# Performance work log

Measured on AMD Instinct MI355X. Metric: run time of the kernel, lower is better.

## Reference

```python
import jax, jax.numpy as jnp
import numpy as np

# Arbitrary non-contiguous kernel tap offsets (constructor arg sk_ind)
SK_IND = np.array([-512, -256, -128, -96, -64, -48, -32, -24, -16, -12, -8, -6,
                   -4, -3, -2, -1, 0, 1, 2, 3, 4, 6, 8, 12, 16, 24, 32, 48,
                   64, 96, 128, 256], dtype=np.int32)
IN_CHANNELS = 64
OUT_CHANNELS = 64
BATCH = 16
INPUT_LEN = 4096


def setup_inputs() -> dict:
    key = jax.random.key(0)
    k1, k2 = jax.random.split(key)
    x = jax.random.normal(k1, (BATCH, IN_CHANNELS, INPUT_LEN), dtype=jnp.float32)
    sk_weights = jax.random.normal(k2, (OUT_CHANNELS, IN_CHANNELS, SK_IND.shape[0]), dtype=jnp.float32)
    return {"x": x, "sk_weights": sk_weights}


def reference(x, sk_weights):
    # x: [B, Cin, L]; sk_weights: [Cout, Cin, K]
    B, C, L = x.shape
    low_pad = max(-int(SK_IND.min()), 0)   # zeros consumed by negative taps
    high_pad = max(int(SK_IND.max()), 0)   # zeros consumed by positive taps
    # Original pads zeros AFTER the signal: [x, zeros(high_pad), zeros(low_pad)];
    # negative numpy indices then wrap into the trailing low_pad zeros.
    padded = jnp.concatenate([x, jnp.zeros((B, C, high_pad + low_pad), x.dtype)], axis=-1)
    padded_len = L + high_pad + low_pad
    idx = SK_IND[:, None] + np.arange(L)                 # [K, L], static
    idx = np.where(idx < 0, padded_len + idx, idx)       # emulate numpy negative-index wrap
    gathered = padded[:, :, idx]                          # [B, Cin, K, L]
    # Per-position GEMM: contract over (Cin, K)
    return jnp.einsum('oik,bikl->bol', sk_weights, gathered)  # [B, Cout, L]
```

## Files before the change

kernel.cpp:

```cpp
#include <hip/hip_runtime.h>


#define B_    16
#define CIN   64
#define COUT  64
#define LEN   4096
#define PAD_LO 512
#define PAD_HI 256
#define LPAD  (LEN + PAD_LO + PAD_HI)
#define NTAP  32

typedef float f32x4 __attribute__((ext_vector_type(4)));
typedef short bf16x8_s __attribute__((ext_vector_type(8)));
typedef __bf16 bf16x8_b __attribute__((ext_vector_type(8)));
typedef unsigned short u16x8 __attribute__((ext_vector_type(8)));

template <typename V>
static __device__ inline auto mfma_16x16x32_bf16(V a, V b, f32x4 c, int)
    -> decltype(__builtin_amdgcn_mfma_f32_16x16x32_bf16(a, b, c, 0, 0, 0)) {
  return __builtin_amdgcn_mfma_f32_16x16x32_bf16(a, b, c, 0, 0, 0);
}
template <typename V>
static __device__ inline f32x4 mfma_16x16x32_bf16(V a, V b, f32x4 c, long) {
  return __builtin_amdgcn_mfma_f32_16x16x32_bf16(
      __builtin_bit_cast(bf16x8_b, a), __builtin_bit_cast(bf16x8_b, b), c, 0, 0, 0);
}

static __device__ inline unsigned short f32_to_bf16_rne(float f) {
  unsigned int u = __builtin_bit_cast(unsigned int, f);
  u += 0x7fffu + ((u >> 16) & 1u);
  return (unsigned short)(u >> 16);
}

static __device__ inline void async_copy16(const void* g, void* l) {
  __builtin_amdgcn_global_load_lds((const __attribute__((address_space(1))) unsigned int*)g,
                                   (__attribute__((address_space(3))) unsigned int*)l, 16, 0, 0);
}

__global__ __launch_bounds__(256) void prep_xw(const float* __restrict__ x,
                                               const float* __restrict__ w,
                                               unsigned short* __restrict__ xp,
                                               unsigned short* __restrict__ wf) {
  __shared__ float tile[64][65];
  const int id = blockIdx.x;
  const int b = 2 * (id & 7) + ((id >> 3) & 1);
  const int xt = id >> 4;
  const int lp0 = xt * 64;
  const int tid = threadIdx.x;
  const bool data = (lp0 >= PAD_LO) && (lp0 < PAD_LO + LEN);
  if (data) {
    const int l0 = lp0 - PAD_LO;
#pragma unroll
    for (int it = 0; it < 4; ++it) {
      const int pidx = it * 256 + tid;
      const int il = pidx >> 4;
      const int lq = (pidx & 15) * 4;
      const float4 v = *(const float4*)&x[(size_t)(b * CIN + il) * LEN + l0 + lq];
      tile[lq + 0][il] = v.x;
      tile[lq + 1][il] = v.y;
      tile[lq + 2][il] = v.z;
      tile[lq + 3][il] = v.w;
    }
  } else if (lp0 < PAD_LO) {
    const int base = (b * 8 + xt) * 1024;
#pragma unroll
    for (int it = 0; it < 4; ++it) {
      const int e = base + it * 256 + tid;
      const int j = e & 7;
      const int lane = (e >> 3) & 63;
      const int m = (e >> 9) & 3;
      const int c = (e >> 11) & 1;
      const int t = e >> 12;
      const int o = m * 16 + (lane & 15);
      const int i = c * 32 + (lane >> 4) * 8 + j;
      wf[e] = f32_to_bf16_rne(w[(size_t)(o * CIN + i) * NTAP + t]);
    }
  }
  __syncthreads();
#pragma unroll
  for (int it = 0; it < 2; ++it) {
    const int pidx = it * 256 + tid;
    const int ll = pidx >> 3;
    const int i8 = (pidx & 7) * 8;
    u16x8 v = {0, 0, 0, 0, 0, 0, 0, 0};
    if (data) {
#pragma unroll
      for (int j = 0; j < 8; ++j) v[j] = f32_to_bf16_rne(tile[ll][i8 + j]);
    }
    *(u16x8*)&xp[(size_t)(b * LPAD + lp0 + ll) * CIN + i8] = v;
  }
}

__global__ __launch_bounds__(512, 2) void sconv_main(const unsigned short* __restrict__ xp,
                                                     const unsigned short* __restrict__ wf,
                                                     float* __restrict__ out) {
  constexpr int TAP[NTAP] = {-512, -256, -128, -96, -64, -48, -32, -24, -16, -12, -8,
                             -6,   -4,   -3,   -2,  -1,  0,   1,   2,   3,   4,  6,
                             8,    12,   16,   24,  32,  48,  64,  96,  128, 256};
  __shared__ alignas(16) char smem[131072];

  const int id = blockIdx.x;
  const int b = (id & 7) * 2 + (id >> 7);
  const int l0 = ((id >> 3) & 15) * 256;
  const int lb = l0 + PAD_LO;
  const int tid = threadIdx.x;
  const int wv = tid >> 6, lane = tid & 63;
  const int q = lane >> 4, r = lane & 15;
  const int lh = wv >> 1, ch = wv & 1;

  const char* xbase = (const char*)xp + ((size_t)b * LPAD + lb) * (CIN * 2);
  const char* wbase = (const char*)wf;

  bf16x8_s Wreg[2][4], Breg[2][4];
  f32x4 acc[4][4] = {};

  auto loadW = [&](int tt, int p) {
    const char* src = wbase + tt * 8192 + ch * 4096 + lane * 16;
#pragma unroll
    for (int m = 0; m < 4; ++m)
      Wreg[p][m] = *(const bf16x8_s*)(src + m * 1024);
  };
  auto readB = [&](int tt, int p) {
    const int e = (TAP[tt] + r) & 7;
#pragma unroll
    for (int n = 0; n < 4; ++n) {
      const int slot = (lb + TAP[tt] + lh * 64 + 16 * n + r) & 1023;
      Breg[p][n] = *(const bf16x8_s*)(smem + slot * 128 + (((ch * 4 + q) ^ e) << 4));
    }
  };

#pragma unroll
  for (int i = 0; i < 16; ++i) {
    const int g = wv + i * 8;
    const int ra = -512 + g * 8 + (lane >> 3);
    const int cs = (lane & 7) ^ (ra & 7);
    const int sb = (lb - 512 + g * 8) & 1023;
    async_copy16(xbase + (ptrdiff_t)ra * 128 + cs * 16, smem + sb * 128);
  }
  loadW(0, 0);
  __syncthreads();
  readB(0, 0);

#pragma unroll
  for (int t = 0; t < NTAP; ++t) {
    const int p = t & 1;
    if (t + 1 < NTAP) {
      loadW(t + 1, p ^ 1);
      readB(t + 1, p ^ 1);
    }
    __builtin_amdgcn_sched_barrier(0);
#pragma unroll
    for (int m = 0; m < 4; ++m)
#pragma unroll
      for (int n = 0; n < 4; ++n)
        acc[m][n] = mfma_16x16x32_bf16(Wreg[p][m], Breg[p][n], acc[m][n], 0);
  }

  __syncthreads();
  if (ch == 1) {
#pragma unroll
    for (int m = 0; m < 4; ++m)
#pragma unroll
      for (int n = 0; n < 4; ++n)
        *(f32x4*)(smem + lh * 16384 + ((m * 4 + n) * 64 + lane) * 16) = acc[m][n];
  }
  __syncthreads();
  if (ch == 0) {
#pragma unroll
    for (int m = 0; m < 4; ++m)
#pragma unroll
      for (int n = 0; n < 4; ++n) {
        const f32x4 other = *(const f32x4*)(smem + lh * 16384 + ((m * 4 + n) * 64 + lane) * 16);
        const f32x4 v = acc[m][n] + other;
#pragma unroll
        for (int d = 0; d < 4; ++d) {
          const int o = 16 * m + 4 * q + d;
          const int l = l0 + lh * 64 + 16 * n + r;
          out[((size_t)b * COUT + o) * LEN + l] = v[d];
        }
      }
  }
}

extern "C" void kernel_launch(void* const* d_in, const int* in_sizes, int n_in,
                              void* d_out, int out_size, void* d_ws, size_t ws_size,
                              hipStream_t stream) {
  const float* x = (const float*)d_in[0];
  const float* w = (const float*)d_in[1];
  float* out = (float*)d_out;

  unsigned short* xp = (unsigned short*)d_ws;
  unsigned short* wfp = xp + (size_t)B_ * LPAD * CIN;

  prep_xw<<<dim3((LPAD / 64) * B_), 256, 0, stream>>>(x, w, xp, wfp);
  sconv_main<<<dim3(256), 512, 0, stream>>>(xp, wfp, out);
}
```

Before: 88.93 us.

## Fuse x transpose and bf16 conversion into main conv kernel staging

The padded, transposed bf16 copy of x is no longer built in the prep kernel. The main kernel now reads fp32 x directly, converts it to bf16 and writes the swizzled LDS window itself, zero-filling out-of-range rows. Part of the staging (rows ahead of the window) is interleaved with the first tap iterations and followed by a barrier. This removes a full global write and re-read of the transposed x buffer, in exchange for synchronous scalar LDS stores and fp32 loads inside the main kernel.

```diff
diff --git a/kernel.cpp b/kernel.cpp
--- a/kernel.cpp
+++ b/kernel.cpp
@@ -5,15 +5,11 @@
 #define CIN   64
 #define COUT  64
 #define LEN   4096
-#define PAD_LO 512
-#define PAD_HI 256
-#define LPAD  (LEN + PAD_LO + PAD_HI)
 #define NTAP  32
 
 typedef float f32x4 __attribute__((ext_vector_type(4)));
 typedef short bf16x8_s __attribute__((ext_vector_type(8)));
 typedef __bf16 bf16x8_b __attribute__((ext_vector_type(8)));
-typedef unsigned short u16x8 __attribute__((ext_vector_type(8)));
 
 template <typename V>
 static __device__ inline auto mfma_16x16x32_bf16(V a, V b, f32x4 c, int)
@@ -32,66 +28,24 @@
   return (unsigned short)(u >> 16);
 }
 
-static __device__ inline void async_copy16(const void* g, void* l) {
-  __builtin_amdgcn_global_load_lds((const __attribute__((address_space(1))) unsigned int*)g,
-                                   (__attribute__((address_space(3))) unsigned int*)l, 16, 0, 0);
-}
-
-__global__ __launch_bounds__(256) void prep_xw(const float* __restrict__ x,
-                                               const float* __restrict__ w,
-                                               unsigned short* __restrict__ xp,
-                                               unsigned short* __restrict__ wf) {
-  __shared__ float tile[64][65];
-  const int id = blockIdx.x;
-  const int b = 2 * (id & 7) + ((id >> 3) & 1);
-  const int xt = id >> 4;
-  const int lp0 = xt * 64;
-  const int tid = threadIdx.x;
-  const bool data = (lp0 >= PAD_LO) && (lp0 < PAD_LO + LEN);
-  if (data) {
-    const int l0 = lp0 - PAD_LO;
+__global__ __launch_bounds__(256) void prep_w(const float* __restrict__ w,
+                                              unsigned short* __restrict__ wf) {
+  const int base = blockIdx.x * 1024;
 #pragma unroll
-    for (int it = 0; it < 4; ++it) {
-      const int pidx = it * 256 + tid;
-      const int il = pidx >> 4;
-      const int lq = (pidx & 15) * 4;
-      const float4 v = *(const float4*)&x[(size_t)(b * CIN + il) * LEN + l0 + lq];
-      tile[lq + 0][il] = v.x;
-      tile[lq + 1][il] = v.y;
-      tile[lq + 2][il] = v.z;
-      tile[lq + 3][il] = v.w;
-    }
-  } else if (lp0 < PAD_LO) {
-    const int base = (b * 8 + xt) * 1024;
-#pragma unroll
-    for (int it = 0; it < 4; ++it) {
-      const int e = base + it * 256 + tid;
-      const int j = e & 7;
-      const int lane = (e >> 3) & 63;
-      const int m = (e >> 9) & 3;
-      const int c = (e >> 11) & 1;
-      const int t = e >> 12;
-      const int o = m * 16 + (lane & 15);
-      const int i = c * 32 + (lane >> 4) * 8 + j;
-      wf[e] = f32_to_bf16_rne(w[(size_t)(o * CIN + i) * NTAP + t]);
-    }
-  }
-  __syncthreads();
-#pragma unroll
-  for (int it = 0; it < 2; ++it) {
-    const int pidx = it * 256 + tid;
-    const int ll = pidx >> 3;
-    const int i8 = (pidx & 7) * 8;
-    u16x8 v = {0, 0, 0, 0, 0, 0, 0, 0};
-    if (data) {
-#pragma unroll
-      for (int j = 0; j < 8; ++j) v[j] = f32_to_bf16_rne(tile[ll][i8 + j]);
-    }
-    *(u16x8*)&xp[(size_t)(b * LPAD + lp0 + ll) * CIN + i8] = v;
+  for (int it = 0; it < 4; ++it) {
+    const int e = base + it * 256 + threadIdx.x;
+    const int j = e & 7;
+    const int lane = (e >> 3) & 63;
+    const int m = (e >> 9) & 3;
+    const int c = (e >> 11) & 1;
+    const int t = e >> 12;
+    const int o = m * 16 + (lane & 15);
+    const int i = c * 32 + (lane >> 4) * 8 + j;
+    wf[e] = f32_to_bf16_rne(w[(size_t)(o * CIN + i) * NTAP + t]);
   }
 }
 
-__global__ __launch_bounds__(512, 2) void sconv_main(const unsigned short* __restrict__ xp,
+__global__ __launch_bounds__(512, 2) void sconv_main(const float* __restrict__ x,
                                                      const unsigned short* __restrict__ wf,
                                                      float* __restrict__ out) {
   constexpr int TAP[NTAP] = {-512, -256, -128, -96, -64, -48, -32, -24, -16, -12, -8,
@@ -102,14 +56,34 @@
   const int id = blockIdx.x;
   const int b = (id & 7) * 2 + (id >> 7);
   const int l0 = ((id >> 3) & 15) * 256;
-  const int lb = l0 + PAD_LO;
+  const int lb = l0 + 512;
   const int tid = threadIdx.x;
   const int wv = tid >> 6, lane = tid & 63;
   const int q = lane >> 4, r = lane & 15;
   const int lh = wv >> 1, ch = wv & 1;
 
-  const char* xbase = (const char*)xp + ((size_t)b * LPAD + lb) * (CIN * 2);
   const char* wbase = (const char*)wf;
+  const float* xb = x + (size_t)b * CIN * LEN;
+
+  auto stage_iter = [&](int lc) {
+    const int h = lane & 7;
+    const int i0 = 16 * (wv & 3) + 2 * h;
+    const int row0 = lc + ((wv >> 2) << 5) + ((lane >> 3) << 2);
+    const int gl = l0 + row0;
+    f32x4 va = {0.f, 0.f, 0.f, 0.f}, vb = {0.f, 0.f, 0.f, 0.f};
+    if ((unsigned)gl < (unsigned)LEN) {
+      va = *(const f32x4*)&xb[(size_t)i0 * LEN + gl];
+      vb = *(const f32x4*)&xb[(size_t)(i0 + 1) * LEN + gl];
+    }
+#pragma unroll
+    for (int j = 0; j < 4; ++j) {
+      const unsigned u = (unsigned)f32_to_bf16_rne(va[j]) |
+                         ((unsigned)f32_to_bf16_rne(vb[j]) << 16);
+      const int slot = (lb + row0 + j) & 1023;
+      const int cs = (i0 >> 3) ^ (slot & 7);
+      *(unsigned*)(smem + slot * 128 + (cs << 4) + (i0 & 7) * 2) = u;
+    }
+  };
 
   bf16x8_s Wreg[2][4], Breg[2][4];
   f32x4 acc[4][4] = {};
@@ -129,21 +103,17 @@
     }
   };
 
-#pragma unroll
-  for (int i = 0; i < 16; ++i) {
-    const int g = wv + i * 8;
-    const int ra = -512 + g * 8 + (lane >> 3);
-    const int cs = (lane & 7) ^ (ra & 7);
-    const int sb = (lb - 512 + g * 8) & 1023;
-    async_copy16(xbase + (ptrdiff_t)ra * 128 + cs * 16, smem + sb * 128);
-  }
   loadW(0, 0);
+#pragma unroll 4
+  for (int k = 0; k < 12; ++k) stage_iter(-512 + k * 64);
   __syncthreads();
   readB(0, 0);
 
 #pragma unroll
   for (int t = 0; t < NTAP; ++t) {
     const int p = t & 1;
+    if (t < 4) stage_iter(256 + t * 64);
+    if (t == 6) __syncthreads();
     if (t + 1 < NTAP) {
       loadW(t + 1, p ^ 1);
       readB(t + 1, p ^ 1);
@@ -189,9 +159,8 @@
   const float* w = (const float*)d_in[1];
   float* out = (float*)d_out;
 
-  unsigned short* xp = (unsigned short*)d_ws;
-  unsigned short* wfp = xp + (size_t)B_ * LPAD * CIN;
+  unsigned short* wfp = (unsigned short*)d_ws;
 
-  prep_xw<<<dim3((LPAD / 64) * B_), 256, 0, stream>>>(x, w, xp, wfp);
-  sconv_main<<<dim3(256), 512, 0, stream>>>(xp, wfp, out);
+  prep_w<<<dim3(128), 256, 0, stream>>>(w, wfp);
+  sconv_main<<<dim3(256), 512, 0, stream>>>(x, wfp, out);
 }
```

Measured after the change: 89.36 us. Within noise of the previous version (+0.5%).
